# Optimization experiments

Measured on AMD Instinct MI355X. Metric: run time of the kernel, lower is better.

## Reference

```python
import jax, jax.numpy as jnp
import numpy as np

N, IN_CH, OUT_CH, E = 100000, 256, 8, 6400000

def setup_inputs() -> dict:
    key = jax.random.key(0)
    k1, k2, k3, k4 = jax.random.split(key, 4)
    X = jax.random.normal(k1, (N, IN_CH), dtype=jnp.float32)
    edge_index = jax.random.randint(k2, (2, E), 0, N, dtype=jnp.int64)
    # torch Linear weights: [out_channels, in_channels], no bias
    W1 = jax.random.normal(k3, (OUT_CH, IN_CH), dtype=jnp.float32) / np.sqrt(IN_CH)
    W2 = jax.random.normal(k4, (OUT_CH, IN_CH), dtype=jnp.float32) / np.sqrt(IN_CH)
    return {"X": X, "edge_index": edge_index, "W1": W1, "W2": W2}

def reference(X, edge_index, W1, W2):
    # Project first ([N, out] is tiny), then gather -- same math as
    # W1(X[e0]) + W2(X[e1]) but avoids two [E, in_channels] intermediates.
    P1 = X @ W1.T  # [N, out]
    P2 = X @ W2.T  # [N, out]
    return P1[edge_index[0]] + P2[edge_index[1]]  # [E, out]
```

## Files before the change

### kernel.cpp

```cpp
#include <hip/hip_runtime.h>
#include <hip/hip_fp16.h>

#define IN_CH 256
#define OUT_CH 8
#define CHUNK 32
#define NCHUNK (IN_CH / CHUNK)
#define ROWSTRIDE 36

typedef float f32x4 __attribute__((ext_vector_type(4)));

__device__ __forceinline__ unsigned pack2h(float a, float b) {
    __half2 h = __floats2half2_rn(a, b);
    return *(unsigned*)&h;
}

__global__ __launch_bounds__(256) void proj_kernel(
    const float* __restrict__ X,
    const float* __restrict__ W1,
    const float* __restrict__ W2,
    uint4* __restrict__ P1v,
    uint4* __restrict__ P2v,
    int n)
{
    __shared__ float Xs[4][64][ROWSTRIDE];

    const int wave = threadIdx.x >> 6;
    const int lane = threadIdx.x & 63;
    const int base = blockIdx.x * 256 + wave * 64;
    if (base >= n) return;

    const bool full = (base + 64 <= n);

    float acc1[OUT_CH];
    float acc2[OUT_CH];
    #pragma unroll
    for (int o = 0; o < OUT_CH; ++o) { acc1[o] = 0.f; acc2[o] = 0.f; }

    const float4* W1v = (const float4*)W1;
    const float4* W2v = (const float4*)W2;

    for (int c = 0; c < NCHUNK; ++c) {
        #pragma unroll
        for (int j = 0; j < 8; ++j) {
            const int idx = lane + 64 * j;
            const int row = idx >> 3;
            const int q   = idx & 7;
            float4 v = make_float4(0.f, 0.f, 0.f, 0.f);
            if (full || base + row < n)
                v = *(const float4*)(X + (size_t)(base + row) * IN_CH + c * CHUNK + q * 4);
            *(float4*)&Xs[wave][row][q * 4] = v;
        }

        float4 xq[8];
        #pragma unroll
        for (int q = 0; q < 8; ++q)
            xq[q] = *(const float4*)&Xs[wave][lane][q * 4];

        #pragma unroll
        for (int o = 0; o < OUT_CH; ++o) {
            float s1 = 0.f, s2 = 0.f;
            #pragma unroll
            for (int q = 0; q < 8; ++q) {
                float4 w1 = W1v[o * 64 + c * 8 + q];
                float4 w2 = W2v[o * 64 + c * 8 + q];
                float4 x  = xq[q];
                s1 += x.x * w1.x + x.y * w1.y + x.z * w1.z + x.w * w1.w;
                s2 += x.x * w2.x + x.y * w2.y + x.z * w2.z + x.w * w2.w;
            }
            acc1[o] += s1;
            acc2[o] += s2;
        }
    }

    const int node = base + lane;
    if (node < n) {
        uint4 p1, p2;
        p1.x = pack2h(acc1[0], acc1[1]); p1.y = pack2h(acc1[2], acc1[3]);
        p1.z = pack2h(acc1[4], acc1[5]); p1.w = pack2h(acc1[6], acc1[7]);
        p2.x = pack2h(acc2[0], acc2[1]); p2.y = pack2h(acc2[2], acc2[3]);
        p2.z = pack2h(acc2[4], acc2[5]); p2.w = pack2h(acc2[6], acc2[7]);
        P1v[node] = p1;
        P2v[node] = p2;
    }
}

__global__ __launch_bounds__(256) void gather_kernel(
    const int* __restrict__ e0,
    const int* __restrict__ e1,
    const uint4* __restrict__ T1,
    const uint4* __restrict__ T2,
    f32x4* __restrict__ outv,
    int E, int n)
{
    const int stride = gridDim.x * 256;
    const unsigned nmax = (unsigned)(n - 1);
    for (int e = blockIdx.x * 256 + threadIdx.x; e < E; e += stride) {
        unsigned i0 = (unsigned)__builtin_nontemporal_load(e0 + e);
        unsigned i1 = (unsigned)__builtin_nontemporal_load(e1 + e);
        i0 = i0 > nmax ? nmax : i0;
        i1 = i1 > nmax ? nmax : i1;

        uint4 a = T1[i0];
        uint4 b = T2[i1];
        const __half2* ah = (const __half2*)&a;
        const __half2* bh = (const __half2*)&b;

        float2 s0 = __half22float2(ah[0]);
        float2 s1 = __half22float2(ah[1]);
        float2 s2 = __half22float2(ah[2]);
        float2 s3 = __half22float2(ah[3]);
        float2 t0 = __half22float2(bh[0]);
        float2 t1 = __half22float2(bh[1]);
        float2 t2 = __half22float2(bh[2]);
        float2 t3 = __half22float2(bh[3]);

        f32x4 r0 = { s0.x + t0.x, s0.y + t0.y, s1.x + t1.x, s1.y + t1.y };
        f32x4 r1 = { s2.x + t2.x, s2.y + t2.y, s3.x + t3.x, s3.y + t3.y };

        size_t oi = 2u * (size_t)e;
        __builtin_nontemporal_store(r0, outv + oi);
        __builtin_nontemporal_store(r1, outv + oi + 1);
    }
}

extern "C" void kernel_launch(void* const* d_in, const int* in_sizes, int n_in,
                              void* d_out, int out_size, void* d_ws, size_t ws_size,
                              hipStream_t stream) {
    const float* X    = (const float*)d_in[0];
    const int*   eidx = (const int*)d_in[1];
    const float* W1   = (const float*)d_in[2];
    const float* W2   = (const float*)d_in[3];

    const int n = in_sizes[0] / IN_CH;
    const int E = in_sizes[1] / 2;

    uint4* P1v = (uint4*)d_ws;
    uint4* P2v = P1v + n;

    const int proj_blocks = (n + 255) / 256;
    proj_kernel<<<proj_blocks, 256, 0, stream>>>(X, W1, W2, P1v, P2v, n);

    const int gather_blocks = (E + 255) / 256;
    gather_kernel<<<gather_blocks, 256, 0, stream>>>(
        eidx, eidx + E, (const uint4*)P1v, (const uint4*)P2v,
        (f32x4*)d_out, E, n);
}
```

Measured before the change: 149.3 us.

## Split projection K-dim across waves and batch four edges per gather thread

The projection kernel now gives each block 64 nodes and has each of its four waves handle one quarter of the input channels. Partial sums are reduced through shared memory, which raises the number of blocks fourfold and shortens each wave's serial loop. The gather kernel now has each thread handle four edges, issuing all index loads and then all table loads up front to expose more memory-level parallelism. The costs are an extra LDS reduction with two barriers in the projection and higher register use in the gather.

Measured after the change: 161.4 us. 8.1% more time.

```diff
diff --git a/kernel.cpp b/kernel.cpp
--- a/kernel.cpp
+++ b/kernel.cpp
@@ -3,9 +3,6 @@
 
 #define IN_CH 256
 #define OUT_CH 8
-#define CHUNK 32
-#define NCHUNK (IN_CH / CHUNK)
-#define ROWSTRIDE 36
 
 typedef float f32x4 __attribute__((ext_vector_type(4)));
 
@@ -18,28 +15,28 @@
     const float* __restrict__ X,
     const float* __restrict__ W1,
     const float* __restrict__ W2,
-    uint4* __restrict__ P1v,
-    uint4* __restrict__ P2v,
+    uint2* __restrict__ P1v,
+    uint2* __restrict__ P2v,
     int n)
 {
-    __shared__ float Xs[4][64][ROWSTRIDE];
+    __shared__ float Xs[4][64][36];
 
-    const int wave = threadIdx.x >> 6;
-    const int lane = threadIdx.x & 63;
-    const int base = blockIdx.x * 256 + wave * 64;
-    if (base >= n) return;
+    const int tid     = threadIdx.x;
+    const int wave    = tid >> 6;
+    const int lane    = tid & 63;
+    const int quarter = __builtin_amdgcn_readfirstlane(wave);
+    const int base    = blockIdx.x * 64;
+    const bool full   = (base + 64 <= n);
 
-    const bool full = (base + 64 <= n);
-
-    float acc1[OUT_CH];
-    float acc2[OUT_CH];
+    float acc[16];
     #pragma unroll
-    for (int o = 0; o < OUT_CH; ++o) { acc1[o] = 0.f; acc2[o] = 0.f; }
+    for (int k = 0; k < 16; ++k) acc[k] = 0.f;
 
     const float4* W1v = (const float4*)W1;
     const float4* W2v = (const float4*)W2;
 
-    for (int c = 0; c < NCHUNK; ++c) {
+    #pragma unroll
+    for (int ch = 0; ch < 2; ++ch) {
         #pragma unroll
         for (int j = 0; j < 8; ++j) {
             const int idx = lane + 64 * j;
@@ -47,7 +44,8 @@
             const int q   = idx & 7;
             float4 v = make_float4(0.f, 0.f, 0.f, 0.f);
             if (full || base + row < n)
-                v = *(const float4*)(X + (size_t)(base + row) * IN_CH + c * CHUNK + q * 4);
+                v = *(const float4*)(X + (size_t)(base + row) * IN_CH
+                                       + quarter * 64 + ch * 32 + q * 4);
             *(float4*)&Xs[wave][row][q * 4] = v;
         }
 
@@ -61,27 +59,57 @@
             float s1 = 0.f, s2 = 0.f;
             #pragma unroll
             for (int q = 0; q < 8; ++q) {
-                float4 w1 = W1v[o * 64 + c * 8 + q];
-                float4 w2 = W2v[o * 64 + c * 8 + q];
+                float4 w1 = W1v[o * 64 + quarter * 16 + ch * 8 + q];
+                float4 w2 = W2v[o * 64 + quarter * 16 + ch * 8 + q];
                 float4 x  = xq[q];
                 s1 += x.x * w1.x + x.y * w1.y + x.z * w1.z + x.w * w1.w;
                 s2 += x.x * w2.x + x.y * w2.y + x.z * w2.z + x.w * w2.w;
             }
-            acc1[o] += s1;
-            acc2[o] += s2;
+            acc[o]     += s1;
+            acc[8 + o] += s2;
         }
     }
 
-    const int node = base + lane;
-    if (node < n) {
-        uint4 p1, p2;
-        p1.x = pack2h(acc1[0], acc1[1]); p1.y = pack2h(acc1[2], acc1[3]);
-        p1.z = pack2h(acc1[4], acc1[5]); p1.w = pack2h(acc1[6], acc1[7]);
-        p2.x = pack2h(acc2[0], acc2[1]); p2.y = pack2h(acc2[2], acc2[3]);
-        p2.z = pack2h(acc2[4], acc2[5]); p2.w = pack2h(acc2[6], acc2[7]);
-        P1v[node] = p1;
-        P2v[node] = p2;
+    __syncthreads();
+    float* Pr = &Xs[0][0][0];
+    #pragma unroll
+    for (int k = 0; k < 16; ++k)
+        Pr[(wave * 64 + lane) * 17 + k] = acc[k];
+    __syncthreads();
+
+    const int node  = tid >> 2;
+    const int g     = tid & 3;
+    const int gnode = base + node;
+    if (gnode < n) {
+        float r0 = 0.f, r1 = 0.f, r2 = 0.f, r3 = 0.f;
+        #pragma unroll
+        for (int w = 0; w < 4; ++w) {
+            const float* p = &Pr[(w * 64 + node) * 17 + g * 4];
+            r0 += p[0]; r1 += p[1]; r2 += p[2]; r3 += p[3];
+        }
+        uint2 val;
+        val.x = pack2h(r0, r1);
+        val.y = pack2h(r2, r3);
+        uint2* dst = (g < 2) ? (P1v + (size_t)gnode * 2 + g)
+                             : (P2v + (size_t)gnode * 2 + (g - 2));
+        *dst = val;
     }
+}
+
+__device__ __forceinline__ void addh8(const uint4 a, const uint4 b,
+                                      f32x4& r0, f32x4& r1) {
+    const __half2* ah = (const __half2*)&a;
+    const __half2* bh = (const __half2*)&b;
+    float2 s0 = __half22float2(ah[0]);
+    float2 s1 = __half22float2(ah[1]);
+    float2 s2 = __half22float2(ah[2]);
+    float2 s3 = __half22float2(ah[3]);
+    float2 t0 = __half22float2(bh[0]);
+    float2 t1 = __half22float2(bh[1]);
+    float2 t2 = __half22float2(bh[2]);
+    float2 t3 = __half22float2(bh[3]);
+    r0 = (f32x4){ s0.x + t0.x, s0.y + t0.y, s1.x + t1.x, s1.y + t1.y };
+    r1 = (f32x4){ s2.x + t2.x, s2.y + t2.y, s3.x + t3.x, s3.y + t3.y };
 }
 
 __global__ __launch_bounds__(256) void gather_kernel(
@@ -92,34 +120,46 @@
     f32x4* __restrict__ outv,
     int E, int n)
 {
-    const int stride = gridDim.x * 256;
+    const int tid  = threadIdx.x;
+    const int base = blockIdx.x * 1024;
     const unsigned nmax = (unsigned)(n - 1);
-    for (int e = blockIdx.x * 256 + threadIdx.x; e < E; e += stride) {
-        unsigned i0 = (unsigned)__builtin_nontemporal_load(e0 + e);
-        unsigned i1 = (unsigned)__builtin_nontemporal_load(e1 + e);
-        i0 = i0 > nmax ? nmax : i0;
-        i1 = i1 > nmax ? nmax : i1;
 
-        uint4 a = T1[i0];
-        uint4 b = T2[i1];
-        const __half2* ah = (const __half2*)&a;
-        const __half2* bh = (const __half2*)&b;
-
-        float2 s0 = __half22float2(ah[0]);
-        float2 s1 = __half22float2(ah[1]);
-        float2 s2 = __half22float2(ah[2]);
-        float2 s3 = __half22float2(ah[3]);
-        float2 t0 = __half22float2(bh[0]);
-        float2 t1 = __half22float2(bh[1]);
-        float2 t2 = __half22float2(bh[2]);
-        float2 t3 = __half22float2(bh[3]);
-
-        f32x4 r0 = { s0.x + t0.x, s0.y + t0.y, s1.x + t1.x, s1.y + t1.y };
-        f32x4 r1 = { s2.x + t2.x, s2.y + t2.y, s3.x + t3.x, s3.y + t3.y };
-
-        size_t oi = 2u * (size_t)e;
-        __builtin_nontemporal_store(r0, outv + oi);
-        __builtin_nontemporal_store(r1, outv + oi + 1);
+    if (base + 1024 <= E) {
+        unsigned i0[4], i1[4];
+        #pragma unroll
+        for (int k = 0; k < 4; ++k) {
+            const int ek = base + k * 256 + tid;
+            i0[k] = (unsigned)__builtin_nontemporal_load(e0 + ek);
+            i1[k] = (unsigned)__builtin_nontemporal_load(e1 + ek);
+        }
+        uint4 a[4], b[4];
+        #pragma unroll
+        for (int k = 0; k < 4; ++k) {
+            a[k] = T1[i0[k] > nmax ? nmax : i0[k]];
+            b[k] = T2[i1[k] > nmax ? nmax : i1[k]];
+        }
+        #pragma unroll
+        for (int k = 0; k < 4; ++k) {
+            f32x4 r0, r1;
+            addh8(a[k], b[k], r0, r1);
+            const size_t oi = 2u * (size_t)(base + k * 256 + tid);
+            __builtin_nontemporal_store(r0, outv + oi);
+            __builtin_nontemporal_store(r1, outv + oi + 1);
+        }
+    } else {
+        for (int k = 0; k < 4; ++k) {
+            const int ek = base + k * 256 + tid;
+            if (ek >= E) break;
+            unsigned i0 = (unsigned)__builtin_nontemporal_load(e0 + ek);
+            unsigned i1 = (unsigned)__builtin_nontemporal_load(e1 + ek);
+            uint4 a = T1[i0 > nmax ? nmax : i0];
+            uint4 b = T2[i1 > nmax ? nmax : i1];
+            f32x4 r0, r1;
+            addh8(a, b, r0, r1);
+            const size_t oi = 2u * (size_t)ek;
+            __builtin_nontemporal_store(r0, outv + oi);
+            __builtin_nontemporal_store(r1, outv + oi + 1);
+        }
     }
 }
 
@@ -134,13 +174,13 @@
     const int n = in_sizes[0] / IN_CH;
     const int E = in_sizes[1] / 2;
 
-    uint4* P1v = (uint4*)d_ws;
-    uint4* P2v = P1v + n;
+    uint2* P1v = (uint2*)d_ws;
+    uint2* P2v = P1v + (size_t)n * 2;
 
-    const int proj_blocks = (n + 255) / 256;
+    const int proj_blocks = (n + 63) / 64;
     proj_kernel<<<proj_blocks, 256, 0, stream>>>(X, W1, W2, P1v, P2v, n);
 
-    const int gather_blocks = (E + 255) / 256;
+    const int gather_blocks = (E + 1023) / 1024;
     gather_kernel<<<gather_blocks, 256, 0, stream>>>(
         eidx, eidx + E, (const uint4*)P1v, (const uint4*)P2v,
         (f32x4*)d_out, E, n);
```
